# Kernel tuning notes

Hardware: AMD Instinct MI355X
Metric: run time of the kernel (lower is better)

## Reference

```python
import jax, jax.numpy as jnp
import numpy as np

B, T, D, U, A, QH = 4096, 128, 64, 64, 8, 64
UNFOLDS = 6
EPS = 1e-8


def setup_inputs() -> dict:
    key = jax.random.key(0)
    ks = jax.random.split(key, 16)
    u = lambda k, s, lo, hi: jax.random.uniform(k, s, jnp.float32, lo, hi)
    return {
        "obs": jax.random.normal(ks[0], (B, T, D), jnp.float32),
        "input_w": jnp.ones((D,), jnp.float32),
        "input_b": jnp.zeros((D,), jnp.float32),
        "sensory_mu": u(ks[1], (D, U), 0.3, 0.8),
        "sensory_sigma": u(ks[2], (D, U), 3.0, 8.0),
        "sensory_w": u(ks[3], (D, U), 0.001, 1.0),
        "sensory_erev": jnp.sign(u(ks[4], (D, U), -1.0, 1.0)),
        "mu": u(ks[5], (U, U), 0.3, 0.8),
        "sigma": u(ks[6], (U, U), 3.0, 8.0),
        "w": u(ks[7], (U, U), 0.001, 1.0),
        "erev": jnp.sign(u(ks[8], (U, U), -1.0, 1.0)),
        "gleak": u(ks[9], (U,), 0.001, 1.0),
        "vleak": u(ks[10], (U,), -0.2, 0.2),
        "cm": u(ks[11], (U,), 0.4, 0.6),
        "W1": jax.random.normal(ks[12], (U, QH), jnp.float32) / np.sqrt(U),
        "b1": jnp.zeros((QH,), jnp.float32),
        "W2": jax.random.normal(ks[13], (QH, A), jnp.float32) / np.sqrt(QH),
        "b2": jnp.zeros((A,), jnp.float32),
    }


def reference(obs, input_w, input_b, sensory_mu, sensory_sigma, sensory_w,
              sensory_erev, mu, sigma, w, erev, gleak, vleak, cm,
              W1, b1, W2, b2):
    sp = jax.nn.softplus
    w_p = sp(w)            # (U, U) positive synapse weights
    sw_p = sp(sensory_w)   # (D, U)
    gl = sp(gleak)         # (U,)
    cm_t = sp(cm) * UNFOLDS  # cm / (elapsed_time / ode_unfolds), elapsed_time = 1.0

    def cell(v, x):
        # x: (B, D) observation at one timestep, v: (B, U) hidden state
        xi = x * input_w + input_b  # affine input mapping
        # sensory synapse activations: (B, D, U)
        s_act = sw_p * jax.nn.sigmoid(sensory_sigma * (xi[:, :, None] - sensory_mu))
        w_num_s = jnp.sum(s_act * sensory_erev, axis=1)  # (B, U)
        w_den_s = jnp.sum(s_act, axis=1)                 # (B, U)
        for _ in range(UNFOLDS):
            # recurrent synapse activations: (B, U, U)
            act = w_p * jax.nn.sigmoid(sigma * (v[:, :, None] - mu))
            num = cm_t * v + gl * vleak + jnp.sum(act * erev, axis=1) + w_num_s
            den = cm_t + gl + jnp.sum(act, axis=1) + w_den_s
            v = num / (den + EPS)
        return v, None

    v0 = jnp.zeros((obs.shape[0], U), obs.dtype)
    hidden, _ = jax.lax.scan(cell, v0, jnp.swapaxes(obs, 0, 1))  # scan over time
    q = jax.nn.relu(hidden @ W1 + b1) @ W2 + b2  # (B, A)
    return q, hidden
```

## Files before the change

kernel.cpp:

```cpp
#include <hip/hip_runtime.h>
#include <math.h>


namespace {

constexpr int kB = 4096, kT = 128, kD = 64, kU = 64, kA = 8, kQH = 64, kUnf = 6;
constexpr float kEps = 1e-8f;
constexpr float kLog2e = 1.4426950408889634f;
constexpr int kWaves = 4;
constexpr int kEPW = 4;
constexpr int kBlock = kWaves * 64;
constexpr int kBPB = kWaves * kEPW;

#if __has_builtin(__builtin_amdgcn_exp2f)
#define EXP2F(x) __builtin_amdgcn_exp2f(x)
#else
#define EXP2F(x) exp2f(x)
#endif

__device__ __forceinline__ float rcp_fast(float x) {
  return __builtin_amdgcn_rcpf(x);
}

__device__ __forceinline__ float bcast(float x, int l) {
  return __int_as_float(__builtin_amdgcn_readlane(__float_as_int(x), l));
}

__device__ __forceinline__ float softplus(float x) { return log1pf(expf(x)); }

__global__ __launch_bounds__(kBlock, 1)
void ltc_fused(const float* __restrict__ obs, const float* __restrict__ input_w,
               const float* __restrict__ input_b, const float* __restrict__ s_mu,
               const float* __restrict__ s_sigma, const float* __restrict__ s_w,
               const float* __restrict__ s_erev, const float* __restrict__ r_mu,
               const float* __restrict__ r_sigma, const float* __restrict__ r_w,
               const float* __restrict__ r_erev, const float* __restrict__ gleak,
               const float* __restrict__ vleak, const float* __restrict__ cm,
               const float* __restrict__ W1, const float* __restrict__ b1,
               const float* __restrict__ W2, const float* __restrict__ b2,
               float* __restrict__ q_out, float* __restrict__ h_out) {
  __shared__ float4 sp[kD * kU];
  __shared__ float4 rp[kU * kU];

  const int tid = threadIdx.x;
  for (int idx = tid; idx < kD * kU; idx += kBlock) {
    const float sg = s_sigma[idx];
    const float swa = softplus(s_w[idx]);
    sp[idx] = make_float4(-kLog2e * sg, kLog2e * sg * s_mu[idx],
                          swa * s_erev[idx], swa);
    const float rg = r_sigma[idx];
    const float rwa = softplus(r_w[idx]);
    rp[idx] = make_float4(-kLog2e * rg, kLog2e * rg * r_mu[idx],
                          rwa * r_erev[idx], rwa);
  }
  __syncthreads();

  const int lane = tid & 63;
  const int wid = tid >> 6;
  const int b0 = (blockIdx.x * kWaves + wid) * kEPW;

  const float gl   = softplus(gleak[lane]);
  const float glvl = gl * vleak[lane];
  const float cmt  = softplus(cm[lane]) * (float)kUnf;
  const float iw   = input_w[lane];
  const float ib   = input_b[lane];

  const float* ob[kEPW];
#pragma unroll
  for (int e = 0; e < kEPW; ++e) ob[e] = obs + (size_t)(b0 + e) * kT * kD;

  float v[kEPW], o[kEPW];
#pragma unroll
  for (int e = 0; e < kEPW; ++e) {
    v[e] = 0.0f;
    o[e] = ob[e][lane];
  }

#pragma unroll 1
  for (int t = 0; t < kT; ++t) {
    const int tn = (t + 1 < kT) ? (t + 1) : t;
    float nx[kEPW];
#pragma unroll
    for (int e = 0; e < kEPW; ++e) nx[e] = ob[e][tn * kD + lane];

    float xi[kEPW];
#pragma unroll
    for (int e = 0; e < kEPW; ++e) xi[e] = fmaf(o[e], iw, ib);

    float ns[kEPW], ds[kEPW];
#pragma unroll
    for (int e = 0; e < kEPW; ++e) { ns[e] = 0.0f; ds[e] = 0.0f; }
#pragma unroll 16
    for (int d = 0; d < kD; ++d) {
      const float4 p = sp[d * kU + lane];
#pragma unroll
      for (int e = 0; e < kEPW; ++e) {
        const float xd = bcast(xi[e], d);
        const float ex = EXP2F(fmaf(p.x, xd, p.y));
        const float g = rcp_fast(1.0f + ex);
        ns[e] = fmaf(g, p.z, ns[e]);
        ds[e] = fmaf(g, p.w, ds[e]);
      }
    }

#pragma unroll 1
    for (int u = 0; u < kUnf; ++u) {
      float num[kEPW], den[kEPW];
#pragma unroll
      for (int e = 0; e < kEPW; ++e) { num[e] = 0.0f; den[e] = 0.0f; }
#pragma unroll 16
      for (int j = 0; j < kU; ++j) {
        const float4 p = rp[j * kU + lane];
#pragma unroll
        for (int e = 0; e < kEPW; ++e) {
          const float vj = bcast(v[e], j);
          const float ex = EXP2F(fmaf(p.x, vj, p.y));
          const float g = rcp_fast(1.0f + ex);
          num[e] = fmaf(g, p.z, num[e]);
          den[e] = fmaf(g, p.w, den[e]);
        }
      }
#pragma unroll
      for (int e = 0; e < kEPW; ++e) {
        const float nt = fmaf(cmt, v[e], glvl) + num[e] + ns[e];
        const float dt = cmt + gl + den[e] + ds[e] + kEps;
        v[e] = nt * rcp_fast(dt);
      }
    }

#pragma unroll
    for (int e = 0; e < kEPW; ++e) o[e] = nx[e];
  }

#pragma unroll
  for (int e = 0; e < kEPW; ++e) h_out[(size_t)(b0 + e) * kU + lane] = v[e];

  float h1[kEPW];
#pragma unroll
  for (int e = 0; e < kEPW; ++e) h1[e] = b1[lane];
#pragma unroll 16
  for (int j = 0; j < kU; ++j) {
    const float w1 = W1[j * kQH + lane];
#pragma unroll
    for (int e = 0; e < kEPW; ++e) h1[e] = fmaf(bcast(v[e], j), w1, h1[e]);
  }
#pragma unroll
  for (int e = 0; e < kEPW; ++e) h1[e] = fmaxf(h1[e], 0.0f);

  float qa[kEPW][kA];
#pragma unroll
  for (int a = 0; a < kA; ++a) {
    const float w2 = W2[lane * kA + a];
#pragma unroll
    for (int e = 0; e < kEPW; ++e) qa[e][a] = h1[e] * w2;
  }
#pragma unroll
  for (int s = 32; s > 0; s >>= 1) {
#pragma unroll
    for (int a = 0; a < kA; ++a) {
#pragma unroll
      for (int e = 0; e < kEPW; ++e) qa[e][a] += __shfl_xor(qa[e][a], s, 64);
    }
  }
  if (lane == 0) {
#pragma unroll
    for (int a = 0; a < kA; ++a) {
#pragma unroll
      for (int e = 0; e < kEPW; ++e) {
        q_out[(size_t)(b0 + e) * kA + a] = qa[e][a] + b2[a];
      }
    }
  }
}

}

extern "C" void kernel_launch(void* const* d_in, const int* in_sizes, int n_in,
                              void* d_out, int out_size, void* d_ws, size_t ws_size,
                              hipStream_t stream) {
  const float* obs     = (const float*)d_in[0];
  const float* input_w = (const float*)d_in[1];
  const float* input_b = (const float*)d_in[2];
  const float* s_mu    = (const float*)d_in[3];
  const float* s_sigma = (const float*)d_in[4];
  const float* s_w     = (const float*)d_in[5];
  const float* s_erev  = (const float*)d_in[6];
  const float* r_mu    = (const float*)d_in[7];
  const float* r_sigma = (const float*)d_in[8];
  const float* r_w     = (const float*)d_in[9];
  const float* r_erev  = (const float*)d_in[10];
  const float* gleak   = (const float*)d_in[11];
  const float* vleak   = (const float*)d_in[12];
  const float* cm      = (const float*)d_in[13];
  const float* W1      = (const float*)d_in[14];
  const float* b1      = (const float*)d_in[15];
  const float* W2      = (const float*)d_in[16];
  const float* b2      = (const float*)d_in[17];

  float* q_out = (float*)d_out;
  float* h_out = q_out + (size_t)kB * kA;

  hipLaunchKernelGGL(ltc_fused, dim3(kB / kBPB), dim3(kBlock), 0, stream,
                     obs, input_w, input_b, s_mu, s_sigma, s_w, s_erev,
                     r_mu, r_sigma, r_w, r_erev, gleak, vleak, cm,
                     W1, b1, W2, b2, q_out, h_out);
}
```

Measured before the change: 3.976 ms.

## Pair sigmoid reciprocals and rebalance waves per block

Computes two sigmoids with a single reciprocal by inverting the product of their denominators, replacing one transcendental rcp per pair with a few multiplies; the exponent is clamped to avoid overflow of the product. Also switches to 8 waves with 2 batch elements each and allows 2 blocks per CU, trading per-wave ILP for more occupancy. The clamp slightly alters results for extreme inputs, and fewer elements per wave reduces the amortisation of LDS parameter loads.

New measurement: 4.228 ms. 1.06x slower.

```diff
diff --git a/kernel.cpp b/kernel.cpp
--- a/kernel.cpp
+++ b/kernel.cpp
@@ -7,8 +7,9 @@
 constexpr int kB = 4096, kT = 128, kD = 64, kU = 64, kA = 8, kQH = 64, kUnf = 6;
 constexpr float kEps = 1e-8f;
 constexpr float kLog2e = 1.4426950408889634f;
-constexpr int kWaves = 4;
-constexpr int kEPW = 4;
+constexpr float kZClamp = 60.0f;
+constexpr int kWaves = 8;
+constexpr int kEPW = 2;
 constexpr int kBlock = kWaves * 64;
 constexpr int kBPB = kWaves * kEPW;
 
@@ -28,7 +29,7 @@
 
 __device__ __forceinline__ float softplus(float x) { return log1pf(expf(x)); }
 
-__global__ __launch_bounds__(kBlock, 1)
+__global__ __launch_bounds__(kBlock, 2)
 void ltc_fused(const float* __restrict__ obs, const float* __restrict__ input_w,
                const float* __restrict__ input_b, const float* __restrict__ s_mu,
                const float* __restrict__ s_sigma, const float* __restrict__ s_w,
@@ -90,16 +91,25 @@
     float ns[kEPW], ds[kEPW];
 #pragma unroll
     for (int e = 0; e < kEPW; ++e) { ns[e] = 0.0f; ds[e] = 0.0f; }
-#pragma unroll 16
-    for (int d = 0; d < kD; ++d) {
-      const float4 p = sp[d * kU + lane];
+#pragma unroll 8
+    for (int d = 0; d < kD; d += 2) {
+      const float4 pA = sp[d * kU + lane];
+      const float4 pB = sp[(d + 1) * kU + lane];
 #pragma unroll
       for (int e = 0; e < kEPW; ++e) {
-        const float xd = bcast(xi[e], d);
-        const float ex = EXP2F(fmaf(p.x, xd, p.y));
-        const float g = rcp_fast(1.0f + ex);
-        ns[e] = fmaf(g, p.z, ns[e]);
-        ds[e] = fmaf(g, p.w, ds[e]);
+        const float xA = bcast(xi[e], d);
+        const float xB = bcast(xi[e], d + 1);
+        const float zA = fminf(fmaf(pA.x, xA, pA.y), kZClamp);
+        const float zB = fminf(fmaf(pB.x, xB, pB.y), kZClamp);
+        const float dA = 1.0f + EXP2F(zA);
+        const float dB = 1.0f + EXP2F(zB);
+        const float R = rcp_fast(dA * dB);
+        const float gA = dB * R;
+        const float gB = dA * R;
+        ns[e] = fmaf(gA, pA.z, ns[e]);
+        ds[e] = fmaf(gA, pA.w, ds[e]);
+        ns[e] = fmaf(gB, pB.z, ns[e]);
+        ds[e] = fmaf(gB, pB.w, ds[e]);
       }
     }
 
@@ -108,16 +118,25 @@
       float num[kEPW], den[kEPW];
 #pragma unroll
       for (int e = 0; e < kEPW; ++e) { num[e] = 0.0f; den[e] = 0.0f; }
-#pragma unroll 16
-      for (int j = 0; j < kU; ++j) {
-        const float4 p = rp[j * kU + lane];
+#pragma unroll 8
+      for (int j = 0; j < kU; j += 2) {
+        const float4 pA = rp[j * kU + lane];
+        const float4 pB = rp[(j + 1) * kU + lane];
 #pragma unroll
         for (int e = 0; e < kEPW; ++e) {
-          const float vj = bcast(v[e], j);
-          const float ex = EXP2F(fmaf(p.x, vj, p.y));
-          const float g = rcp_fast(1.0f + ex);
-          num[e] = fmaf(g, p.z, num[e]);
-          den[e] = fmaf(g, p.w, den[e]);
+          const float vA = bcast(v[e], j);
+          const float vB = bcast(v[e], j + 1);
+          const float zA = fminf(fmaf(pA.x, vA, pA.y), kZClamp);
+          const float zB = fminf(fmaf(pB.x, vB, pB.y), kZClamp);
+          const float dA = 1.0f + EXP2F(zA);
+          const float dB = 1.0f + EXP2F(zB);
+          const float R = rcp_fast(dA * dB);
+          const float gA = dB * R;
+          const float gB = dA * R;
+          num[e] = fmaf(gA, pA.z, num[e]);
+          den[e] = fmaf(gA, pA.w, den[e]);
+          num[e] = fmaf(gB, pB.z, num[e]);
+          den[e] = fmaf(gB, pB.w, den[e]);
         }
       }
 #pragma unroll
```
